# Kernel optimization log

Measured on AMD Instinct MI355X. Metric: run time of the kernel, lower is better.

Reference implementation:

```python
import jax, jax.numpy as jnp
import numpy as np
from jax import lax

B, N, F, H = 128, 512, 16, 128
HIST, FW, E = 24, 24, 8192


def setup_inputs() -> dict:
    key = jax.random.key(0)
    ks = jax.random.split(key, 12)
    feature = jax.random.normal(ks[0], (B, HIST + FW, N, F), dtype=jnp.float32)
    pm25_hist = jax.random.normal(ks[1], (B, HIST, N, 1), dtype=jnp.float32)
    # base edges within one graph of N nodes, tiled per batch with node offsets
    base = jax.random.randint(ks[2], (2, E), 0, N)
    offs = (jnp.arange(B) * N).astype(jnp.int32)
    edge_index = (base[:, None, :] + offs[None, :, None]).reshape(2, B * E)
    s = 0.05
    W_nb = jax.random.normal(ks[3], (1, F + 1), dtype=jnp.float32) * s
    b_nb = jnp.zeros((1,), dtype=jnp.float32)
    W_root = jax.random.normal(ks[4], (1, F + 1), dtype=jnp.float32) * s
    W_ih = jax.random.normal(ks[5], (3 * H, F + 2), dtype=jnp.float32) * s
    W_hh = jax.random.normal(ks[6], (3 * H, H), dtype=jnp.float32) * s
    b_ih = jax.random.normal(ks[7], (3 * H,), dtype=jnp.float32) * s
    b_hh = jax.random.normal(ks[8], (3 * H,), dtype=jnp.float32) * s
    W_out = jax.random.normal(ks[9], (1, H), dtype=jnp.float32) * s
    b_out = jnp.zeros((1,), dtype=jnp.float32)
    return {"feature": feature, "pm25_hist": pm25_hist, "edge_index": edge_index,
            "W_nb": W_nb, "b_nb": b_nb, "W_root": W_root,
            "W_ih": W_ih, "W_hh": W_hh, "b_ih": b_ih, "b_hh": b_hh,
            "W_out": W_out, "b_out": b_out}


def _forward(feature, pm25_hist, edge_index, W_nb, b_nb, W_root,
             W_ih, W_hh, b_ih, b_hh, W_out, b_out):
    src, dst = edge_index[0], edge_index[1]
    BN = B * N
    # mean-aggregation denominator (in-degree, clamped at 1), constant over steps
    deg = jax.ops.segment_sum(jnp.ones_like(dst, dtype=jnp.float32), dst,
                              num_segments=BN)
    inv_deg = 1.0 / jnp.maximum(deg, 1.0)

    h0 = jnp.zeros((BN, H), dtype=feature.dtype)
    xn0 = pm25_hist[:, -1]  # (B, N, 1)

    def step(carry, feat_t):
        hn, xn = carry
        x = jnp.concatenate([xn, feat_t], axis=-1)          # (B, N, F+1)
        xg = x.reshape(BN, F + 1)
        # SAGEConv (mean aggr): W_nb @ mean(x_j) + b_nb + W_root @ x_i
        msg = xg[src]                                        # (B*E, F+1) gather
        agg = jax.ops.segment_sum(msg, dst, num_segments=BN) * inv_deg[:, None]
        gcn = jax.nn.sigmoid(agg @ W_nb.T + b_nb + xg @ W_root.T)  # (BN, 1)
        x2 = jnp.concatenate([xg, gcn], axis=-1)             # (BN, F+2)
        # torch GRUCell: gate order r, z, n
        gi = x2 @ W_ih.T + b_ih
        gh = hn @ W_hh.T + b_hh
        i_r, i_z, i_n = jnp.split(gi, 3, axis=-1)
        h_r, h_z, h_n = jnp.split(gh, 3, axis=-1)
        r = jax.nn.sigmoid(i_r + h_r)
        z = jax.nn.sigmoid(i_z + h_z)
        n = jnp.tanh(i_n + r * h_n)
        hn_new = (1.0 - z) * n + z * hn                      # (BN, H)
        xn_new = hn_new.reshape(B, N, H) @ W_out.T + b_out   # (B, N, 1)
        return (hn_new, xn_new), xn_new

    feat_seq = jnp.transpose(feature[:, HIST:], (1, 0, 2, 3))  # (FW, B, N, F)
    _, preds = lax.scan(step, (h0, xn0), feat_seq)             # (FW, B, N, 1)
    return jnp.transpose(preds, (1, 0, 2, 3))                  # (B, FW, N, 1)


def reference(feature, pm25_hist, edge_index, W_nb, b_nb, W_root,
              W_ih, W_hh, b_ih, b_hh, W_out, b_out):
    return _forward(feature, pm25_hist, edge_index, W_nb, b_nb, W_root,
                    W_ih, W_hh, b_ih, b_hh, W_out, b_out)
```

## Files before the change

kernel.cpp:

```cpp
#include <hip/hip_runtime.h>

typedef short bf16x8 __attribute__((ext_vector_type(8)));
typedef float f32x4  __attribute__((ext_vector_type(4)));

#define Bb 128
#define Nn 512
#define Ff 16
#define Hh 128
#define HIST 24
#define FW 24
#define Ee 8192
#define BN (Bb*Nn)
#define NE (Bb*Ee)
#define THIST (HIST+FW)
#define MB 64
#define NSLOT 20
#define WPN (4*4*2*NSLOT*16*8)

__device__ __forceinline__ unsigned short f2bfu(float x){
  union { float f; unsigned u; } v; v.f = x;
  unsigned r = v.u + 0x7FFFu + ((v.u >> 16) & 1u);
  return (unsigned short)(r >> 16);
}
__device__ __forceinline__ float sigm(float x){ return 1.f/(1.f + __expf(-x)); }
__device__ __forceinline__ float tanh_f(float x){ return 1.f - 2.f/(__expf(2.f*x) + 1.f); }

__global__ __launch_bounds__(512) void k_csr(const int* __restrict__ eidx, int* __restrict__ rowptrL,
                                             int* __restrict__ srcsL, float* __restrict__ invdegL){
  __shared__ int cnt[512];
  __shared__ int scan[512];
  int tid = threadIdx.x;
  cnt[tid] = 0;
  __syncthreads();
  for (int e = tid; e < Ee; e += 512) atomicAdd(&cnt[eidx[NE + e]], 1);
  __syncthreads();
  int c = cnt[tid];
  scan[tid] = c;
  __syncthreads();
  for (int off = 1; off < 512; off <<= 1){
    int v = (tid >= off) ? scan[tid-off] : 0;
    __syncthreads();
    scan[tid] += v;
    __syncthreads();
  }
  int excl = scan[tid] - c;
  rowptrL[tid] = excl;
  if (tid == 0) rowptrL[512] = Ee;
  invdegL[tid] = 1.0f / fmaxf((float)c, 1.0f);
  __syncthreads();
  scan[tid] = excl;
  cnt[tid] = 0;
  __syncthreads();
  for (int e = tid; e < Ee; e += 512){
    int d = eidx[NE + e];
    int pos = scan[d] + atomicAdd(&cnt[d], 1);
    srcsL[pos] = eidx[e];
  }
}

__global__ __launch_bounds__(256) void k_init_xn(const float* __restrict__ pm, float* __restrict__ xn){
  int g = blockIdx.x*256 + threadIdx.x;
  if (g < BN){ int b = g>>9, n = g&511; xn[g] = pm[((size_t)b*HIST + (HIST-1))*Nn + n]; }
}

__global__ __launch_bounds__(256) void k_wpack(const float* __restrict__ W_ih, const float* __restrict__ W_hh,
                                               unsigned short* __restrict__ Wpack){
  int idx = blockIdx.x*256 + threadIdx.x;
  if (idx >= WPN) return;
  int j = idx & 7;
  int r = idx >> 3;
  int c = r & 15; r >>= 4;
  int slot = r % NSLOT; r /= NSLOT;
  int nt = r & 1; r >>= 1;
  int w = r & 3; int g = r >> 2;
  int k = slot*8 + j;
  int col = w*32 + nt*16 + c;
  float v = 0.f;
  if (g == 0 || g == 1){
    int row = (g == 0) ? col : 128 + col;
    if (k < 32){ if (k < 18) v = W_ih[row*18 + k]; }
    else v = W_hh[(size_t)row*128 + (k-32)];
  } else if (g == 2){
    if (k < 18) v = W_ih[(256+col)*18 + k];
  } else {
    if (k >= 32) v = W_hh[(size_t)(256+col)*128 + (k-32)];
  }
  Wpack[idx] = f2bfu(v);
}

__global__ __launch_bounds__(256) void k_sfeat(const float* __restrict__ feature, const float* __restrict__ W_nb,
                                               const float* __restrict__ W_root,
                                               float* __restrict__ sfeat, float* __restrict__ rootf,
                                               unsigned short* __restrict__ xfb){
  int idx = blockIdx.x*256 + threadIdx.x;
  if (idx >= FW*BN) return;
  int t = idx >> 16, g = idx & 0xFFFF;
  int b = g>>9, n = g&511;
  const float* f = feature + (((size_t)b*THIST + HIST + t)*Nn + n)*Ff;
  unsigned short xv[16];
  float s = 0.f, r = 0.f;
  #pragma unroll
  for (int k = 0; k < Ff; k++){
    float v = f[k];
    s = fmaf(v, W_nb[1+k], s); r = fmaf(v, W_root[1+k], r);
    xv[k] = f2bfu(v);
  }
  sfeat[idx] = s; rootf[idx] = r;
  *(bf16x8*)&xfb[(size_t)idx*16]     = *(bf16x8*)&xv[0];
  *(bf16x8*)&xfb[(size_t)idx*16 + 8] = *(bf16x8*)&xv[8];
}

__global__ __launch_bounds__(256) void k_aggT(const int* __restrict__ rowptrL, const int* __restrict__ srcsL,
                                              const float* __restrict__ sfeat, const float* __restrict__ invdegL,
                                              const float* __restrict__ b_nb, float* __restrict__ pre){
  int idx = blockIdx.x*256 + threadIdx.x;
  if (idx >= FW*BN) return;
  int g = idx & 0xFFFF, t = idx >> 16;
  int n = g & 511, b = g >> 9;
  int e0 = rowptrL[n], e1 = rowptrL[n+1];
  const float* sf = sfeat + (size_t)t*BN + (size_t)b*Nn;
  float s = 0.f;
  for (int e = e0; e < e1; e++) s += sf[srcsL[e]];
  pre[idx] = invdegL[n]*s + pre[idx] + b_nb[0];
}

__global__ __launch_bounds__(256, 2) void k_gru(
    float* __restrict__ h,
    const float* __restrict__ xn_in, float* __restrict__ xn_out,
    const float* __restrict__ pre_t, const float* __restrict__ invdegL,
    const unsigned short* __restrict__ xfb_t,
    const int* __restrict__ rowptrL, const int* __restrict__ srcsL,
    const unsigned short* __restrict__ Wpack,
    const float* __restrict__ b_ih, const float* __restrict__ b_hh,
    const float* __restrict__ W_nb, const float* __restrict__ W_root,
    const float* __restrict__ W_out, const float* __restrict__ b_out,
    float* __restrict__ out, int t)
{
  __shared__ __align__(16) short A_lds[NSLOT*MB*8];
  __shared__ float gcn_lds[MB], xn_lds[MB];
  __shared__ float xnpart[4][MB];
  const int tid = threadIdx.x;
  const int g0 = blockIdx.x * MB;
  const int b = g0 >> 9, n0 = g0 & 511;

  {
    int m = tid >> 2, sub = tid & 3;
    int n = n0 + m;
    int e1 = rowptrL[n+1];
    const float* xb = xn_in + (size_t)b*Nn;
    float sx = 0.f;
    for (int e = rowptrL[n] + sub; e < e1; e += 4) sx += xb[srcsL[e]];
    sx += __shfl_xor(sx, 1); sx += __shfl_xor(sx, 2);
    if (sub == 0){
      int g = g0 + m;
      float xv = xn_in[g];
      float prea = pre_t[g] + invdegL[n]*W_nb[0]*sx + W_root[0]*xv;
      xn_lds[m] = xv;
      gcn_lds[m] = sigm(prea);
    }
  }
  __syncthreads();

  if (tid < MB){
    int row = tid;
    const bf16x8* xf = (const bf16x8*)&xfb_t[(size_t)(g0+row)*16];
    bf16x8 x0 = xf[0], x1 = xf[1];
    short v[32];
    v[0] = (short)f2bfu(xn_lds[row]);
    #pragma unroll
    for (int k = 0; k < 8; k++){ v[1+k] = x0[k]; v[9+k] = x1[k]; }
    v[17] = (short)f2bfu(gcn_lds[row]);
    #pragma unroll
    for (int k = 18; k < 32; k++) v[k] = 0;
    #pragma unroll
    for (int s = 0; s < 4; s++){
      int pos = (row + s) & 63;
      *(bf16x8*)&A_lds[(s*MB + pos)*8] = *(bf16x8*)&v[s*8];
    }
  }
  for (int i = tid; i < MB*16; i += 256){
    int kg = i & 15, row = i >> 4;
    const float4* hp = (const float4*)&h[(size_t)(g0+row)*Hh + kg*8];
    float4 h0 = hp[0], h1 = hp[1];
    short hv[8];
    hv[0]=(short)f2bfu(h0.x); hv[1]=(short)f2bfu(h0.y); hv[2]=(short)f2bfu(h0.z); hv[3]=(short)f2bfu(h0.w);
    hv[4]=(short)f2bfu(h1.x); hv[5]=(short)f2bfu(h1.y); hv[6]=(short)f2bfu(h1.z); hv[7]=(short)f2bfu(h1.w);
    int s = 4 + kg, pos = (row + s) & 63;
    *(bf16x8*)&A_lds[(s*MB + pos)*8] = *(bf16x8*)&hv[0];
  }
  __syncthreads();

  const int l = tid & 63, w = tid >> 6;
  const int c = l & 15, lg = l >> 4;

  f32x4 acc[4][4][2] = {};
  #pragma unroll
  for (int kk = 0; kk < 5; kk++){
    bf16x8 a[4];
    #pragma unroll
    for (int m = 0; m < 4; m++){
      int s = kk*4 + lg, row = m*16 + c, pos = (row + s) & 63;
      a[m] = *(const bf16x8*)&A_lds[(s*MB + pos)*8];
    }
    #pragma unroll
    for (int g = 0; g < 4; g++){
      #pragma unroll
      for (int nt = 0; nt < 2; nt++){
        const bf16x8 bv = *(const bf16x8*)&Wpack[ (size_t)((((g*4+w)*2+nt)*NSLOT + kk*4 + lg)*16 + c)*8 ];
        #pragma unroll
        for (int m = 0; m < 4; m++)
          acc[g][m][nt] = __builtin_amdgcn_mfma_f32_16x16x32_bf16(a[m], bv, acc[g][m][nt], 0, 0, 0);
      }
    }
  }

  float bR[2], bZ[2], bI[2], bH[2], wo[2]; int jj[2];
  #pragma unroll
  for (int nt = 0; nt < 2; nt++){
    int j = w*32 + nt*16 + c; jj[nt] = j;
    bR[nt] = b_ih[j] + b_hh[j];
    bZ[nt] = b_ih[128+j] + b_hh[128+j];
    bI[nt] = b_ih[256+j];
    bH[nt] = b_hh[256+j];
    wo[nt] = W_out[j];
  }
  float psum[4][4] = {};
  #pragma unroll
  for (int m = 0; m < 4; m++){
    #pragma unroll
    for (int nt = 0; nt < 2; nt++){
      #pragma unroll
      for (int q = 0; q < 4; q++){
        int row = 16*m + lg*4 + q;
        size_t off = (size_t)(g0 + row)*Hh + jj[nt];
        float hold = h[off];
        float rr = sigm(acc[0][m][nt][q] + bR[nt]);
        float zz = sigm(acc[1][m][nt][q] + bZ[nt]);
        float nn = tanh_f(acc[2][m][nt][q] + bI[nt] + rr*(acc[3][m][nt][q] + bH[nt]));
        float hv = (1.f - zz)*nn + zz*hold;
        h[off] = hv;
        psum[m][q] = fmaf(hv, wo[nt], psum[m][q]);
      }
    }
  }
  #pragma unroll
  for (int mask = 1; mask < 16; mask <<= 1){
    #pragma unroll
    for (int m = 0; m < 4; m++)
      #pragma unroll
      for (int q = 0; q < 4; q++)
        psum[m][q] += __shfl_xor(psum[m][q], mask);
  }
  if (c == 0){
    #pragma unroll
    for (int m = 0; m < 4; m++)
      #pragma unroll
      for (int q = 0; q < 4; q++)
        xnpart[w][16*m + lg*4 + q] = psum[m][q];
  }
  __syncthreads();
  if (tid < MB){
    int row = tid, g = g0 + row, n = n0 + row;
    float xv = xnpart[0][row] + xnpart[1][row] + xnpart[2][row] + xnpart[3][row] + b_out[0];
    xn_out[g] = xv;
    out[((size_t)b*FW + t)*Nn + n] = xv;
  }
}

extern "C" void kernel_launch(void* const* d_in, const int* in_sizes, int n_in,
                              void* d_out, int out_size, void* d_ws, size_t ws_size,
                              hipStream_t stream){
  const float* feature = (const float*)d_in[0];
  const float* pm25    = (const float*)d_in[1];
  const int*   eidx    = (const int*)d_in[2];
  const float* W_nb    = (const float*)d_in[3];
  const float* b_nb    = (const float*)d_in[4];
  const float* W_root  = (const float*)d_in[5];
  const float* W_ih    = (const float*)d_in[6];
  const float* W_hh    = (const float*)d_in[7];
  const float* b_ih    = (const float*)d_in[8];
  const float* b_hh    = (const float*)d_in[9];
  const float* W_out   = (const float*)d_in[10];
  const float* b_out   = (const float*)d_in[11];
  float* out = (float*)d_out;

  char* wsp = (char*)d_ws;
  float* invdegL = (float*)wsp; wsp += 512*4;
  int*   rowptrL = (int*)wsp;   wsp += 520*4;
  int*   srcsL   = (int*)wsp;   wsp += Ee*4;
  float* xn_a    = (float*)wsp; wsp += (size_t)BN*4;
  float* xn_b    = (float*)wsp; wsp += (size_t)BN*4;
  float* sfeat   = (float*)wsp; wsp += (size_t)FW*BN*4;
  float* pre     = (float*)wsp; wsp += (size_t)FW*BN*4;
  unsigned short* xfb = (unsigned short*)wsp; wsp += (size_t)FW*BN*16*2;
  unsigned short* Wpack = (unsigned short*)wsp; wsp += (size_t)WPN*2;
  float* hbuf    = (float*)wsp; wsp += (size_t)BN*Hh*4;

  hipMemsetAsync(hbuf, 0, (size_t)BN*Hh*sizeof(float), stream);

  k_csr    <<<1, 512, 0, stream>>>(eidx, rowptrL, srcsL, invdegL);
  k_init_xn<<<BN/256, 256, 0, stream>>>(pm25, xn_a);
  k_wpack  <<<(WPN+255)/256, 256, 0, stream>>>(W_ih, W_hh, Wpack);
  k_sfeat  <<<(FW*BN)/256, 256, 0, stream>>>(feature, W_nb, W_root, sfeat, pre, xfb);
  k_aggT   <<<(FW*BN)/256, 256, 0, stream>>>(rowptrL, srcsL, sfeat, invdegL, b_nb, pre);

  float* xa = xn_a; float* xb = xn_b;
  for (int t = 0; t < FW; t++){
    k_gru<<<BN/MB, 256, 0, stream>>>(hbuf, xa, xb, pre + (size_t)t*BN, invdegL,
                                     xfb + (size_t)t*BN*16, rowptrL, srcsL, Wpack,
                                     b_ih, b_hh, W_nb, W_root, W_out, b_out, out, t);
    float* tmp = xa; xa = xb; xb = tmp;
  }
}
```

Measured before the change: 1.183 ms.

## Fuse all GRU timesteps into one persistent per-graph kernel with LDS hidden state

Replaces the 24 per-timestep GRU launches with a single kernel of one 512-thread block per graph that loops over all timesteps. The bf16 hidden state stays in LDS with an XOR swizzle, and xn stays in LDS for the graph aggregation, which removes per-step launches and the global h reload/convert. Only 128 blocks run, about 138KB of LDS each, so occupancy is low and the 8 row-tiles are processed serially with several barriers. fp32 h is still written to and read from global every step.

```diff
diff --git a/kernel.cpp b/kernel.cpp
--- a/kernel.cpp
+++ b/kernel.cpp
@@ -13,9 +13,9 @@
 #define BN (Bb*Nn)
 #define NE (Bb*Ee)
 #define THIST (HIST+FW)
-#define MB 64
 #define NSLOT 20
-#define WPN (4*4*2*NSLOT*16*8)
+#define WPN (4*8*NSLOT*16*8)
+#define LDS_BYTES 141312
 
 __device__ __forceinline__ unsigned short f2bfu(float x){
   union { float f; unsigned u; } v; v.f = x;
@@ -56,11 +56,6 @@
     int pos = scan[d] + atomicAdd(&cnt[d], 1);
     srcsL[pos] = eidx[e];
   }
-}
-
-__global__ __launch_bounds__(256) void k_init_xn(const float* __restrict__ pm, float* __restrict__ xn){
-  int g = blockIdx.x*256 + threadIdx.x;
-  if (g < BN){ int b = g>>9, n = g&511; xn[g] = pm[((size_t)b*HIST + (HIST-1))*Nn + n]; }
 }
 
 __global__ __launch_bounds__(256) void k_wpack(const float* __restrict__ W_ih, const float* __restrict__ W_hh,
@@ -71,10 +66,9 @@
   int r = idx >> 3;
   int c = r & 15; r >>= 4;
   int slot = r % NSLOT; r /= NSLOT;
-  int nt = r & 1; r >>= 1;
-  int w = r & 3; int g = r >> 2;
+  int w = r & 7; int g = r >> 3;
   int k = slot*8 + j;
-  int col = w*32 + nt*16 + c;
+  int col = w*16 + c;
   float v = 0.f;
   if (g == 0 || g == 1){
     int row = (g == 0) ? col : 128 + col;
@@ -124,146 +118,148 @@
   pre[idx] = invdegL[n]*s + pre[idx] + b_nb[0];
 }
 
-__global__ __launch_bounds__(256, 2) void k_gru(
-    float* __restrict__ h,
-    const float* __restrict__ xn_in, float* __restrict__ xn_out,
-    const float* __restrict__ pre_t, const float* __restrict__ invdegL,
-    const unsigned short* __restrict__ xfb_t,
+__global__ __launch_bounds__(512, 2) void k_fused(
+    const float* __restrict__ pm, const float* __restrict__ pre,
+    const float* __restrict__ invdegL, const unsigned short* __restrict__ xfb,
     const int* __restrict__ rowptrL, const int* __restrict__ srcsL,
     const unsigned short* __restrict__ Wpack,
     const float* __restrict__ b_ih, const float* __restrict__ b_hh,
     const float* __restrict__ W_nb, const float* __restrict__ W_root,
     const float* __restrict__ W_out, const float* __restrict__ b_out,
-    float* __restrict__ out, int t)
+    float* __restrict__ h_g, float* __restrict__ out)
 {
-  __shared__ __align__(16) short A_lds[NSLOT*MB*8];
-  __shared__ float gcn_lds[MB], xn_lds[MB];
-  __shared__ float xnpart[4][MB];
+  extern __shared__ char smem[];
+  short* h_lds  = (short*)smem;
+  short* x2_lds = (short*)(smem + 131072);
+  float* xn_lds = (float*)(smem + 135168);
+  float* xnpart = (float*)(smem + 139264);
+
   const int tid = threadIdx.x;
-  const int g0 = blockIdx.x * MB;
-  const int b = g0 >> 9, n0 = g0 & 511;
-
-  {
-    int m = tid >> 2, sub = tid & 3;
-    int n = n0 + m;
-    int e1 = rowptrL[n+1];
-    const float* xb = xn_in + (size_t)b*Nn;
-    float sx = 0.f;
-    for (int e = rowptrL[n] + sub; e < e1; e += 4) sx += xb[srcsL[e]];
-    sx += __shfl_xor(sx, 1); sx += __shfl_xor(sx, 2);
-    if (sub == 0){
-      int g = g0 + m;
-      float xv = xn_in[g];
-      float prea = pre_t[g] + invdegL[n]*W_nb[0]*sx + W_root[0]*xv;
-      xn_lds[m] = xv;
-      gcn_lds[m] = sigm(prea);
-    }
-  }
-  __syncthreads();
-
-  if (tid < MB){
-    int row = tid;
-    const bf16x8* xf = (const bf16x8*)&xfb_t[(size_t)(g0+row)*16];
-    bf16x8 x0 = xf[0], x1 = xf[1];
-    short v[32];
-    v[0] = (short)f2bfu(xn_lds[row]);
-    #pragma unroll
-    for (int k = 0; k < 8; k++){ v[1+k] = x0[k]; v[9+k] = x1[k]; }
-    v[17] = (short)f2bfu(gcn_lds[row]);
-    #pragma unroll
-    for (int k = 18; k < 32; k++) v[k] = 0;
-    #pragma unroll
-    for (int s = 0; s < 4; s++){
-      int pos = (row + s) & 63;
-      *(bf16x8*)&A_lds[(s*MB + pos)*8] = *(bf16x8*)&v[s*8];
-    }
-  }
-  for (int i = tid; i < MB*16; i += 256){
-    int kg = i & 15, row = i >> 4;
-    const float4* hp = (const float4*)&h[(size_t)(g0+row)*Hh + kg*8];
-    float4 h0 = hp[0], h1 = hp[1];
-    short hv[8];
-    hv[0]=(short)f2bfu(h0.x); hv[1]=(short)f2bfu(h0.y); hv[2]=(short)f2bfu(h0.z); hv[3]=(short)f2bfu(h0.w);
-    hv[4]=(short)f2bfu(h1.x); hv[5]=(short)f2bfu(h1.y); hv[6]=(short)f2bfu(h1.z); hv[7]=(short)f2bfu(h1.w);
-    int s = 4 + kg, pos = (row + s) & 63;
-    *(bf16x8*)&A_lds[(s*MB + pos)*8] = *(bf16x8*)&hv[0];
-  }
-  __syncthreads();
-
+  const int b = blockIdx.x;
   const int l = tid & 63, w = tid >> 6;
   const int c = l & 15, lg = l >> 4;
 
-  f32x4 acc[4][4][2] = {};
-  #pragma unroll
-  for (int kk = 0; kk < 5; kk++){
-    bf16x8 a[4];
-    #pragma unroll
-    for (int m = 0; m < 4; m++){
-      int s = kk*4 + lg, row = m*16 + c, pos = (row + s) & 63;
-      a[m] = *(const bf16x8*)&A_lds[(s*MB + pos)*8];
+  {
+    bf16x8 z = {};
+    for (int i = tid; i < 512*128/8; i += 512) ((bf16x8*)h_lds)[i] = z;
+    xn_lds[tid] = pm[((size_t)b*HIST + (HIST-1))*Nn + tid];
+  }
+  __syncthreads();
+
+  const int j = w*16 + c;
+  const float bR = b_ih[j] + b_hh[j];
+  const float bZ = b_ih[128+j] + b_hh[128+j];
+  const float bI = b_ih[256+j];
+  const float bH = b_hh[256+j];
+  const float wo = W_out[j];
+  const float wnb0 = W_nb[0], wrt0 = W_root[0], bo = b_out[0];
+
+  for (int t = 0; t < FW; t++){
+    const float* xn_cur = xn_lds + (t&1)*512;
+    float* xn_nxt = xn_lds + ((t&1)^1)*512;
+    const float* pre_t = pre + (size_t)t*BN + (size_t)b*Nn;
+    const unsigned short* xfb_t = xfb + ((size_t)t*BN + (size_t)b*Nn)*16;
+
+    for (int t8 = 0; t8 < 8; t8++){
+      const int tb = t8*64;
+      {
+        int m = tid >> 3, sub = tid & 7;
+        int n = tb + m;
+        int e0 = rowptrL[n], e1 = rowptrL[n+1];
+        float sx = 0.f;
+        for (int e = e0 + sub; e < e1; e += 8) sx += xn_cur[srcsL[e]];
+        sx += __shfl_xor(sx, 1); sx += __shfl_xor(sx, 2); sx += __shfl_xor(sx, 4);
+        if (sub == 0){
+          float xv = xn_cur[n];
+          float prea = pre_t[n] + invdegL[n]*wnb0*sx + wrt0*xv;
+          float gcn = sigm(prea);
+          const bf16x8* xf = (const bf16x8*)&xfb_t[(size_t)n*16];
+          bf16x8 x0 = xf[0], x1 = xf[1];
+          short v[32];
+          v[0] = (short)f2bfu(xv);
+          #pragma unroll
+          for (int k = 0; k < 8; k++){ v[1+k] = x0[k]; v[9+k] = x1[k]; }
+          v[17] = (short)f2bfu(gcn);
+          #pragma unroll
+          for (int k = 18; k < 32; k++) v[k] = 0;
+          #pragma unroll
+          for (int s = 0; s < 4; s++)
+            *(bf16x8*)&x2_lds[(s*64 + m)*8] = *(bf16x8*)&v[s*8];
+        }
+      }
+      __syncthreads();
+
+      f32x4 acc[4][4] = {};
+      #pragma unroll
+      for (int kk = 0; kk < 5; kk++){
+        bf16x8 a[4];
+        if (kk == 0){
+          #pragma unroll
+          for (int m = 0; m < 4; m++)
+            a[m] = *(const bf16x8*)&x2_lds[(lg*64 + m*16 + c)*8];
+        } else {
+          int sh = (kk-1)*4 + lg;
+          #pragma unroll
+          for (int m = 0; m < 4; m++){
+            int row = tb + m*16 + c;
+            a[m] = *(const bf16x8*)&h_lds[row*128 + ((sh ^ c)*8)];
+          }
+        }
+        #pragma unroll
+        for (int g = 0; g < 4; g++){
+          const bf16x8 bv = *(const bf16x8*)&Wpack[(size_t)(((g*8 + w)*NSLOT + kk*4 + lg)*16 + c)*8];
+          #pragma unroll
+          for (int m = 0; m < 4; m++)
+            acc[g][m] = __builtin_amdgcn_mfma_f32_16x16x32_bf16(a[m], bv, acc[g][m], 0, 0, 0);
+        }
+      }
+      __syncthreads();
+
+      float psum[4][4];
+      #pragma unroll
+      for (int m = 0; m < 4; m++){
+        #pragma unroll
+        for (int q = 0; q < 4; q++){
+          int row = tb + m*16 + lg*4 + q;
+          size_t off = ((size_t)b*Nn + row)*Hh + j;
+          float hold = (t == 0) ? 0.f : h_g[off];
+          float rr = sigm(acc[0][m][q] + bR);
+          float zz = sigm(acc[1][m][q] + bZ);
+          float nn = tanh_f(acc[2][m][q] + bI + rr*(acc[3][m][q] + bH));
+          float hv = (1.f - zz)*nn + zz*hold;
+          h_g[off] = hv;
+          int rl = lg*4 + q;
+          h_lds[row*128 + (((j>>3) ^ rl)*8) + (j&7)] = (short)f2bfu(hv);
+          psum[m][q] = hv * wo;
+        }
+      }
+      #pragma unroll
+      for (int mask = 1; mask < 16; mask <<= 1){
+        #pragma unroll
+        for (int m = 0; m < 4; m++)
+          #pragma unroll
+          for (int q = 0; q < 4; q++)
+            psum[m][q] += __shfl_xor(psum[m][q], mask);
+      }
+      if (c == 0){
+        #pragma unroll
+        for (int m = 0; m < 4; m++)
+          #pragma unroll
+          for (int q = 0; q < 4; q++)
+            xnpart[w*64 + m*16 + lg*4 + q] = psum[m][q];
+      }
+      __syncthreads();
+
+      if (tid < 64){
+        int row = tb + tid;
+        float xv = bo;
+        #pragma unroll
+        for (int ww = 0; ww < 8; ww++) xv += xnpart[ww*64 + tid];
+        xn_nxt[row] = xv;
+        out[((size_t)b*FW + t)*Nn + row] = xv;
+      }
     }
-    #pragma unroll
-    for (int g = 0; g < 4; g++){
-      #pragma unroll
-      for (int nt = 0; nt < 2; nt++){
-        const bf16x8 bv = *(const bf16x8*)&Wpack[ (size_t)((((g*4+w)*2+nt)*NSLOT + kk*4 + lg)*16 + c)*8 ];
-        #pragma unroll
-        for (int m = 0; m < 4; m++)
-          acc[g][m][nt] = __builtin_amdgcn_mfma_f32_16x16x32_bf16(a[m], bv, acc[g][m][nt], 0, 0, 0);
-      }
-    }
-  }
-
-  float bR[2], bZ[2], bI[2], bH[2], wo[2]; int jj[2];
-  #pragma unroll
-  for (int nt = 0; nt < 2; nt++){
-    int j = w*32 + nt*16 + c; jj[nt] = j;
-    bR[nt] = b_ih[j] + b_hh[j];
-    bZ[nt] = b_ih[128+j] + b_hh[128+j];
-    bI[nt] = b_ih[256+j];
-    bH[nt] = b_hh[256+j];
-    wo[nt] = W_out[j];
-  }
-  float psum[4][4] = {};
-  #pragma unroll
-  for (int m = 0; m < 4; m++){
-    #pragma unroll
-    for (int nt = 0; nt < 2; nt++){
-      #pragma unroll
-      for (int q = 0; q < 4; q++){
-        int row = 16*m + lg*4 + q;
-        size_t off = (size_t)(g0 + row)*Hh + jj[nt];
-        float hold = h[off];
-        float rr = sigm(acc[0][m][nt][q] + bR[nt]);
-        float zz = sigm(acc[1][m][nt][q] + bZ[nt]);
-        float nn = tanh_f(acc[2][m][nt][q] + bI[nt] + rr*(acc[3][m][nt][q] + bH[nt]));
-        float hv = (1.f - zz)*nn + zz*hold;
-        h[off] = hv;
-        psum[m][q] = fmaf(hv, wo[nt], psum[m][q]);
-      }
-    }
-  }
-  #pragma unroll
-  for (int mask = 1; mask < 16; mask <<= 1){
-    #pragma unroll
-    for (int m = 0; m < 4; m++)
-      #pragma unroll
-      for (int q = 0; q < 4; q++)
-        psum[m][q] += __shfl_xor(psum[m][q], mask);
-  }
-  if (c == 0){
-    #pragma unroll
-    for (int m = 0; m < 4; m++)
-      #pragma unroll
-      for (int q = 0; q < 4; q++)
-        xnpart[w][16*m + lg*4 + q] = psum[m][q];
-  }
-  __syncthreads();
-  if (tid < MB){
-    int row = tid, g = g0 + row, n = n0 + row;
-    float xv = xnpart[0][row] + xnpart[1][row] + xnpart[2][row] + xnpart[3][row] + b_out[0];
-    xn_out[g] = xv;
-    out[((size_t)b*FW + t)*Nn + n] = xv;
+    __syncthreads();
   }
 }
 
@@ -288,27 +284,23 @@
   float* invdegL = (float*)wsp; wsp += 512*4;
   int*   rowptrL = (int*)wsp;   wsp += 520*4;
   int*   srcsL   = (int*)wsp;   wsp += Ee*4;
-  float* xn_a    = (float*)wsp; wsp += (size_t)BN*4;
-  float* xn_b    = (float*)wsp; wsp += (size_t)BN*4;
   float* sfeat   = (float*)wsp; wsp += (size_t)FW*BN*4;
   float* pre     = (float*)wsp; wsp += (size_t)FW*BN*4;
   unsigned short* xfb = (unsigned short*)wsp; wsp += (size_t)FW*BN*16*2;
   unsigned short* Wpack = (unsigned short*)wsp; wsp += (size_t)WPN*2;
-  float* hbuf    = (float*)wsp; wsp += (size_t)BN*Hh*4;
-
-  hipMemsetAsync(hbuf, 0, (size_t)BN*Hh*sizeof(float), stream);
-
-  k_csr    <<<1, 512, 0, stream>>>(eidx, rowptrL, srcsL, invdegL);
-  k_init_xn<<<BN/256, 256, 0, stream>>>(pm25, xn_a);
-  k_wpack  <<<(WPN+255)/256, 256, 0, stream>>>(W_ih, W_hh, Wpack);
-  k_sfeat  <<<(FW*BN)/256, 256, 0, stream>>>(feature, W_nb, W_root, sfeat, pre, xfb);
-  k_aggT   <<<(FW*BN)/256, 256, 0, stream>>>(rowptrL, srcsL, sfeat, invdegL, b_nb, pre);
-
-  float* xa = xn_a; float* xb = xn_b;
-  for (int t = 0; t < FW; t++){
-    k_gru<<<BN/MB, 256, 0, stream>>>(hbuf, xa, xb, pre + (size_t)t*BN, invdegL,
-                                     xfb + (size_t)t*BN*16, rowptrL, srcsL, Wpack,
-                                     b_ih, b_hh, W_nb, W_root, W_out, b_out, out, t);
-    float* tmp = xa; xa = xb; xb = tmp;
-  }
-}
+  float* h_g     = (float*)wsp; wsp += (size_t)BN*Hh*4;
+
+  static int attr_set = 0;
+  if (!attr_set){
+    hipFuncSetAttribute((const void*)k_fused, hipFuncAttributeMaxDynamicSharedMemorySize, LDS_BYTES);
+    attr_set = 1;
+  }
+
+  k_csr   <<<1, 512, 0, stream>>>(eidx, rowptrL, srcsL, invdegL);
+  k_wpack <<<(WPN+255)/256, 256, 0, stream>>>(W_ih, W_hh, Wpack);
+  k_sfeat <<<(FW*BN)/256, 256, 0, stream>>>(feature, W_nb, W_root, sfeat, pre, xfb);
+  k_aggT  <<<(FW*BN)/256, 256, 0, stream>>>(rowptrL, srcsL, sfeat, invdegL, b_nb, pre);
+
+  k_fused<<<Bb, 512, LDS_BYTES, stream>>>(pm25, pre, invdegL, xfb, rowptrL, srcsL, Wpack,
+                                          b_ih, b_hh, W_nb, W_root, W_out, b_out, h_g, out);
+}
```

New measurement: 1.984 ms. 67.7% more time.
